# Performance work log

Measured on AMD Instinct MI355X. Metric: run time of the kernel, lower is better.

## Reference

```python
import jax, jax.numpy as jnp
import numpy as np

B, S, D, H = 2, 2048, 1024, 16
Dh = D // H

def setup_inputs() -> dict:
    key = jax.random.key(0)
    ks = jax.random.split(key, 11)
    def lin(k, fan_in):
        bound = 1.0 / np.sqrt(fan_in)
        kw, kb = jax.random.split(k)
        W = jax.random.uniform(kw, (D, D), jnp.float32, -bound, bound)
        b = jax.random.uniform(kb, (D,), jnp.float32, -bound, bound)
        return W, b
    Wq, bq = lin(ks[0], D)
    Wk, bk = lin(ks[1], D)
    Wv, bv = lin(ks[2], D)
    Wo, bo = lin(ks[3], D)
    Q = jax.random.normal(ks[4], (B, S, D), jnp.float32)
    K = jax.random.normal(ks[5], (B, S, D), jnp.float32)
    V = jax.random.normal(ks[6], (B, S, D), jnp.float32)
    return {"Q": Q, "K": K, "V": V, "Wq": Wq, "bq": bq, "Wk": Wk, "bk": bk,
            "Wv": Wv, "bv": bv, "Wo": Wo, "bo": bo}

def _split_heads(x):
    # [B,S,D] -> [B,H,S,Dh]
    b, s, _ = x.shape
    return x.reshape(b, s, H, Dh).transpose(0, 2, 1, 3)

def reference(Q, K, V, Wq, bq, Wk, bk, Wv, bv, Wo, bo):
    q = _split_heads(Q @ Wq.T + bq)
    k = _split_heads(K @ Wk.T + bk)
    v = _split_heads(V @ Wv.T + bv)
    scores = jnp.einsum('bhqd,bhkd->bhqk', q, k) / jnp.sqrt(jnp.float32(Dh))
    attn = jax.nn.softmax(scores, axis=-1)
    out = jnp.einsum('bhqk,bhkd->bhqd', attn, v)  # [B,H,S,Dh]
    out = out.transpose(0, 2, 1, 3).reshape(Q.shape[0], Q.shape[1], D)
    return out @ Wo.T + bo
```

## Files before the change

kernel.cpp:

```cpp
#include <hip/hip_runtime.h>

#define SEQ 2048
#define DMODEL 1024
#define NH 16
#define DH 64

typedef __attribute__((ext_vector_type(8))) short bf16x8;
typedef __attribute__((ext_vector_type(4))) short bf16x4;
typedef __attribute__((ext_vector_type(4))) float floatx4;
typedef __attribute__((ext_vector_type(4))) unsigned short u16x4;
typedef unsigned short u16;
typedef unsigned int u32;

typedef const void __attribute__((address_space(1)))* as1cvp;
typedef void __attribute__((address_space(3)))* as3vp;

__device__ __forceinline__ void glds16(const void* g, void* l) {
    __builtin_amdgcn_global_load_lds((as1cvp)g, (as3vp)l, 16, 0, 0);
}

__device__ __forceinline__ u16 f2bf(float f) {
    union { u32 u; float f; } v; v.f = f;
    return (u16)((v.u + 0x8000u) >> 16);
}

__device__ __forceinline__ u32 pk2(float a, float b) {
    union { u32 u; float f; } x, y; x.f = a; y.f = b;
    u32 xr = x.u + 0x8000u, yr = y.u + 0x8000u;
#if __has_builtin(__builtin_amdgcn_perm)
    return __builtin_amdgcn_perm(yr, xr, 0x07060302u);
#else
    return (xr >> 16) | (yr & 0xffff0000u);
#endif
}

__device__ __forceinline__ float ex2(float x) {
#if __has_builtin(__builtin_amdgcn_exp2f)
    return __builtin_amdgcn_exp2f(x);
#else
    float r; asm("v_exp_f32 %0, %1" : "=v"(r) : "v"(x)); return r;
#endif
}

__device__ __forceinline__ floatx4 mfma16(bf16x4 a, bf16x4 b, floatx4 c) {
#if __has_builtin(__builtin_amdgcn_mfma_f32_16x16x16bf16_1k)
    return __builtin_amdgcn_mfma_f32_16x16x16bf16_1k(a, b, c, 0, 0, 0);
#else
    asm volatile("v_mfma_f32_16x16x16_bf16 %0, %1, %2, %0" : "+v"(c) : "v"(a), "v"(b));
    return c;
#endif
}

__device__ __forceinline__ uint4 cvt8(const float* __restrict__ p) {
    float4 a = *(const float4*)p;
    float4 b = *(const float4*)(p + 4);
    uint4 q;
    q.x = pk2(a.x, a.y); q.y = pk2(a.z, a.w);
    q.z = pk2(b.x, b.y); q.w = pk2(b.z, b.w);
    return q;
}

#define QSCALE 0.18033688011112042f

__global__ __launch_bounds__(256) void cvt_all(
    const float* __restrict__ Q, const float* __restrict__ K, const float* __restrict__ V,
    const float* __restrict__ W0, const float* __restrict__ W1,
    const float* __restrict__ W2, const float* __restrict__ W3,
    u16* __restrict__ Qb, u16* __restrict__ Kb, u16* __restrict__ Vb,
    u16* __restrict__ Wb)
{
    const int y = blockIdx.y;
    const float* src; u16* dst;
    if (y == 0)      { src = Q;  dst = Qb; }
    else if (y == 1) { src = K;  dst = Kb; }
    else if (y == 2) { src = V;  dst = Vb; }
    else {
        if (blockIdx.x >= 512) return;
        src = (y == 3) ? W0 : (y == 4) ? W1 : (y == 5) ? W2 : W3;
        dst = Wb + (size_t)(y - 3) * 1048576;
    }
    size_t i = ((size_t)blockIdx.x * 256 + threadIdx.x) * 8;
    *(uint4*)(dst + i) = cvt8(src + i);
}

__global__ __launch_bounds__(256) void cvt_w(
    const float* __restrict__ W0, const float* __restrict__ W1,
    const float* __restrict__ W2, const float* __restrict__ W3,
    u16* __restrict__ out)
{
    const float* src = (blockIdx.y == 0) ? W0 : (blockIdx.y == 1) ? W1
                     : (blockIdx.y == 2) ? W2 : W3;
    size_t i = ((size_t)blockIdx.x * 256 + threadIdx.x) * 8;
    *(uint4*)(out + (size_t)blockIdx.y * 1048576 + i) = cvt8(src + i);
}

__device__ __forceinline__ void qkv_store(
    int z, u16* __restrict__ outp, int rowg, int col, floatx4 a4, float bv, float sc)
{
    union { u32 w[2]; u16 h[4]; u16x4 v4; } pk;
    pk.w[0] = pk2((a4[0] + bv) * sc, (a4[1] + bv) * sc);
    pk.w[1] = pk2((a4[2] + bv) * sc, (a4[3] + bv) * sc);
    int b = rowg >> 11, s = rowg & 2047, h = col >> 6, d = col & 63;
    if (z < 2) {
#pragma unroll
        for (int r = 0; r < 4; r++)
            outp[((size_t)(b * NH + h) * SEQ + s + r) * DH + d] = pk.h[r];
    } else {
        *(u16x4*)(outp + ((size_t)(b * NH + h) * DH + d) * SEQ + s) = pk.v4;
    }
}

__global__ __launch_bounds__(256) void gemm_qkv_bb(
    const u16* __restrict__ Qb, const u16* __restrict__ Kb, const u16* __restrict__ Vb,
    const u16* __restrict__ Wb,
    const float* __restrict__ b0, const float* __restrict__ b1, const float* __restrict__ b2,
    u16* __restrict__ qo, u16* __restrict__ ko, u16* __restrict__ vto)
{
    __shared__ __align__(16) u16 As[128 * 32];
    __shared__ __align__(16) u16 Bs[128 * 32];
    const int tid = threadIdx.x, l = tid & 63, w = tid >> 6;
    const int lm = l & 15, quad = l >> 4;
    const int wr = (w >> 1) * 64, wc = (w & 1) * 64;
    const int bm = blockIdx.y * 128, bn = blockIdx.x * 128;
    const int z = blockIdx.z;
    const u16* A      = (z == 0) ? Qb : (z == 1) ? Kb : Vb;
    const u16* W      = Wb + (size_t)z * 1048576;
    const float* bias = (z == 0) ? b0 : (z == 1) ? b1 : b2;

    const int srow = tid >> 2, scol = (tid & 3) * 8;

    floatx4 acc[4][4];
#pragma unroll
    for (int i = 0; i < 4; i++)
#pragma unroll
        for (int j = 0; j < 4; j++) acc[i][j] = (floatx4){0.f, 0.f, 0.f, 0.f};

    for (int kt = 0; kt < DMODEL; kt += 32) {
        __syncthreads();
        glds16(A + (size_t)(bm + srow) * DMODEL + kt + scol, As + w * 512);
        glds16(A + (size_t)(bm + 64 + srow) * DMODEL + kt + scol, As + 2048 + w * 512);
        glds16(W + (size_t)(bn + srow) * DMODEL + kt + scol, Bs + w * 512);
        glds16(W + (size_t)(bn + 64 + srow) * DMODEL + kt + scol, Bs + 2048 + w * 512);
        __syncthreads();

        bf16x8 af[4], bfr[4];
#pragma unroll
        for (int mi = 0; mi < 4; mi++)
            af[mi] = *(const bf16x8*)(As + (wr + mi * 16 + lm) * 32 + quad * 8);
#pragma unroll
        for (int ni = 0; ni < 4; ni++)
            bfr[ni] = *(const bf16x8*)(Bs + (wc + ni * 16 + lm) * 32 + quad * 8);
#pragma unroll
        for (int mi = 0; mi < 4; mi++)
#pragma unroll
            for (int ni = 0; ni < 4; ni++)
                acc[mi][ni] = __builtin_amdgcn_mfma_f32_16x16x32_bf16(
                    af[mi], bfr[ni], acc[mi][ni], 0, 0, 0);
    }

    const float sc = (z == 0) ? QSCALE : 1.0f;
    u16* outp = (z == 0) ? qo : (z == 1) ? ko : vto;
#pragma unroll
    for (int ni = 0; ni < 4; ni++) {
        int col = bn + wc + ni * 16 + lm;
        float bv = bias[col];
#pragma unroll
        for (int mi = 0; mi < 4; mi++)
            qkv_store(z, outp, bm + wr + mi * 16 + quad * 4, col, acc[mi][ni], bv, sc);
    }
}

template<bool WBF>
__global__ __launch_bounds__(256) void gemm_qkv(
    const float* __restrict__ Qf, const float* __restrict__ Kf, const float* __restrict__ Vf,
    const void* __restrict__ W0, const void* __restrict__ W1, const void* __restrict__ W2,
    const float* __restrict__ b0, const float* __restrict__ b1, const float* __restrict__ b2,
    u16* __restrict__ qo, u16* __restrict__ ko, u16* __restrict__ vto)
{
    __shared__ __align__(16) u16 As[128 * 32];
    __shared__ __align__(16) u16 Bs[128 * 32];
    const int tid = threadIdx.x, l = tid & 63, w = tid >> 6;
    const int lm = l & 15, quad = l >> 4;
    const int wr = (w >> 1) * 64, wc = (w & 1) * 64;
    const int bm = blockIdx.y * 128, bn = blockIdx.x * 128;
    const int z = blockIdx.z;
    const float* A    = (z == 0) ? Qf : (z == 1) ? Kf : Vf;
    const void* Wp    = (z == 0) ? W0 : (z == 1) ? W1 : W2;
    const float* bias = (z == 0) ? b0 : (z == 1) ? b1 : b2;

    floatx4 acc[4][4];
#pragma unroll
    for (int i = 0; i < 4; i++)
#pragma unroll
        for (int j = 0; j < 4; j++) acc[i][j] = (floatx4){0.f, 0.f, 0.f, 0.f};

    for (int kt = 0; kt < DMODEL; kt += 32) {
        __syncthreads();
#pragma unroll
        for (int j = 0; j < 2; j++) {
            int ch = j * 256 + tid, row = ch >> 2, c = ch & 3;
            *(uint4*)(As + ch * 8) = cvt8(A + (size_t)(bm + row) * DMODEL + kt + c * 8);
        }
        if (WBF) {
            const u16* Wb = (const u16*)Wp;
            glds16(Wb + (size_t)(bn + (tid >> 2)) * DMODEL + kt + (tid & 3) * 8, Bs + w * 512);
            glds16(Wb + (size_t)(bn + 64 + (tid >> 2)) * DMODEL + kt + (tid & 3) * 8, Bs + 2048 + w * 512);
        } else {
            const float* Wf = (const float*)Wp;
#pragma unroll
            for (int j = 0; j < 2; j++) {
                int ch = j * 256 + tid, row = ch >> 2, c = ch & 3;
                *(uint4*)(Bs + ch * 8) = cvt8(Wf + (size_t)(bn + row) * DMODEL + kt + c * 8);
            }
        }
        __syncthreads();

        bf16x8 af[4], bfr[4];
#pragma unroll
        for (int mi = 0; mi < 4; mi++)
            af[mi] = *(const bf16x8*)(As + (wr + mi * 16 + lm) * 32 + quad * 8);
#pragma unroll
        for (int ni = 0; ni < 4; ni++)
            bfr[ni] = *(const bf16x8*)(Bs + (wc + ni * 16 + lm) * 32 + quad * 8);
#pragma unroll
        for (int mi = 0; mi < 4; mi++)
#pragma unroll
            for (int ni = 0; ni < 4; ni++)
                acc[mi][ni] = __builtin_amdgcn_mfma_f32_16x16x32_bf16(
                    af[mi], bfr[ni], acc[mi][ni], 0, 0, 0);
    }

    const float sc = (z == 0) ? QSCALE : 1.0f;
    u16* outp = (z == 0) ? qo : (z == 1) ? ko : vto;
#pragma unroll
    for (int ni = 0; ni < 4; ni++) {
        int col = bn + wc + ni * 16 + lm;
        float bv = bias[col];
#pragma unroll
        for (int mi = 0; mi < 4; mi++)
            qkv_store(z, outp, bm + wr + mi * 16 + quad * 4, col, acc[mi][ni], bv, sc);
    }
}

template<bool WBF>
__global__ __launch_bounds__(256) void gemm_o(
    const u16* __restrict__ A, const void* __restrict__ Wp,
    const float* __restrict__ bias, float* __restrict__ out)
{
    __shared__ __align__(16) u16 As[128 * 32];
    __shared__ __align__(16) u16 Bs[64 * 32];
    const int tid = threadIdx.x, l = tid & 63, w = tid >> 6;
    const int lm = l & 15, quad = l >> 4;
    const int bm = blockIdx.y * 128, bn = blockIdx.x * 64;

    floatx4 acc[2][4];
#pragma unroll
    for (int i = 0; i < 2; i++)
#pragma unroll
        for (int j = 0; j < 4; j++) acc[i][j] = (floatx4){0.f, 0.f, 0.f, 0.f};

    for (int kt = 0; kt < DMODEL; kt += 32) {
        __syncthreads();
        glds16(A + (size_t)(bm + (tid >> 2)) * DMODEL + kt + (tid & 3) * 8, As + w * 512);
        glds16(A + (size_t)(bm + 64 + (tid >> 2)) * DMODEL + kt + (tid & 3) * 8, As + 2048 + w * 512);
        if (WBF) {
            glds16((const u16*)Wp + (size_t)(bn + (tid >> 2)) * DMODEL + kt + (tid & 3) * 8, Bs + w * 512);
        } else {
            *(uint4*)(Bs + tid * 8) =
                cvt8((const float*)Wp + (size_t)(bn + (tid >> 2)) * DMODEL + kt + (tid & 3) * 8);
        }
        __syncthreads();

        bf16x8 af[2], bfr[4];
#pragma unroll
        for (int mi = 0; mi < 2; mi++)
            af[mi] = *(const bf16x8*)(As + (w * 32 + mi * 16 + lm) * 32 + quad * 8);
#pragma unroll
        for (int ni = 0; ni < 4; ni++)
            bfr[ni] = *(const bf16x8*)(Bs + (ni * 16 + lm) * 32 + quad * 8);
#pragma unroll
        for (int mi = 0; mi < 2; mi++)
#pragma unroll
            for (int ni = 0; ni < 4; ni++)
                acc[mi][ni] = __builtin_amdgcn_mfma_f32_16x16x32_bf16(
                    af[mi], bfr[ni], acc[mi][ni], 0, 0, 0);
    }

#pragma unroll
    for (int ni = 0; ni < 4; ni++) {
        int col = bn + ni * 16 + lm;
        float bv = bias[col];
#pragma unroll
        for (int mi = 0; mi < 2; mi++) {
#pragma unroll
            for (int r = 0; r < 4; r++) {
                int rowg = bm + w * 32 + mi * 16 + quad * 4 + r;
                out[(size_t)rowg * DMODEL + col] = acc[mi][ni][r] + bv;
            }
        }
    }
}

#define SP 72
__global__ __launch_bounds__(256, 2) void attn_kernel(
    const u16* __restrict__ q, const u16* __restrict__ k,
    const u16* __restrict__ vt, u16* __restrict__ out)
{
    __shared__ __align__(16) u16 Ks[64 * SP];
    __shared__ __align__(16) u16 Vs[64 * SP];
    const int tid = threadIdx.x, l = tid & 63, w = tid >> 6;
    const int lm = l & 15, quad = l >> 4;
    const int qt = blockIdx.x, bh = blockIdx.y;
    const int b = bh >> 4, h = bh & 15;

    bf16x8 qf[2][2];
#pragma unroll
    for (int nt = 0; nt < 2; nt++) {
        int row = qt * 128 + w * 32 + nt * 16 + lm;
        const u16* qp = q + ((size_t)bh * SEQ + row) * DH;
#pragma unroll
        for (int ks = 0; ks < 2; ks++)
            qf[nt][ks] = *(const bf16x8*)(qp + ks * 32 + quad * 8);
    }

    floatx4 O[4][2];
#pragma unroll
    for (int dt = 0; dt < 4; dt++)
#pragma unroll
        for (int nt = 0; nt < 2; nt++) O[dt][nt] = (floatx4){0.f, 0.f, 0.f, 0.f};
    float mrun[2] = {-1e30f, -1e30f}, lrun[2] = {0.f, 0.f};

    const int srow = tid >> 3, scol = (tid & 7) * 8;
    const int pb0 = ((scol >> 2) & 3) * 16 + (scol >> 4) * 4;
    const u16* kbase = k + (size_t)bh * SEQ * DH;
    const u16* vbase = vt + (size_t)bh * DH * SEQ;
    uint4 kr0, kr1, vr0, vr1;
    kr0 = *(const uint4*)(kbase + (size_t)srow * DH + scol);
    kr1 = *(const uint4*)(kbase + (size_t)(srow + 32) * DH + scol);
    vr0 = *(const uint4*)(vbase + (size_t)srow * SEQ + scol);
    vr1 = *(const uint4*)(vbase + (size_t)(srow + 32) * SEQ + scol);

    for (int t = 0; t < SEQ / 64; t++) {
        __syncthreads();
        *(uint4*)(Ks + srow * SP + scol) = kr0;
        *(uint4*)(Ks + (srow + 32) * SP + scol) = kr1;
        *(uint2*)(Vs + srow * SP + pb0)             = make_uint2(vr0.x, vr0.y);
        *(uint2*)(Vs + srow * SP + pb0 + 16)        = make_uint2(vr0.z, vr0.w);
        *(uint2*)(Vs + (srow + 32) * SP + pb0)      = make_uint2(vr1.x, vr1.y);
        *(uint2*)(Vs + (srow + 32) * SP + pb0 + 16) = make_uint2(vr1.z, vr1.w);
        __syncthreads();
        if (t + 1 < SEQ / 64) {
            const u16* kg = kbase + (size_t)(t + 1) * 64 * DH;
            const u16* vg = vbase + (size_t)(t + 1) * 64;
            kr0 = *(const uint4*)(kg + (size_t)srow * DH + scol);
            kr1 = *(const uint4*)(kg + (size_t)(srow + 32) * DH + scol);
            vr0 = *(const uint4*)(vg + (size_t)srow * SEQ + scol);
            vr1 = *(const uint4*)(vg + (size_t)(srow + 32) * SEQ + scol);
        }

        floatx4 Sc[4][2];
#pragma unroll
        for (int mt = 0; mt < 4; mt++) {
            bf16x8 ka0 = *(const bf16x8*)(Ks + (mt * 16 + lm) * SP + quad * 8);
            bf16x8 ka1 = *(const bf16x8*)(Ks + (mt * 16 + lm) * SP + 32 + quad * 8);
#pragma unroll
            for (int nt = 0; nt < 2; nt++) {
                floatx4 c = (floatx4){0.f, 0.f, 0.f, 0.f};
                c = __builtin_amdgcn_mfma_f32_16x16x32_bf16(ka0, qf[nt][0], c, 0, 0, 0);
                c = __builtin_amdgcn_mfma_f32_16x16x32_bf16(ka1, qf[nt][1], c, 0, 0, 0);
                Sc[mt][nt] = c;
            }
        }

        bf16x4 pb[4][2];
#pragma unroll
        for (int nt = 0; nt < 2; nt++) {
            float m0 = -1e30f;
#pragma unroll
            for (int mt = 0; mt < 4; mt++)
#pragma unroll
                for (int r = 0; r < 4; r++) m0 = fmaxf(m0, Sc[mt][nt][r]);
            m0 = fmaxf(m0, __shfl_xor(m0, 16));
            m0 = fmaxf(m0, __shfl_xor(m0, 32));
            if (!__all(m0 <= mrun[nt] + 8.0f)) {
                float mn = fmaxf(mrun[nt], m0);
                float alpha = ex2(mrun[nt] - mn);
                mrun[nt] = mn;
                lrun[nt] *= alpha;
#pragma unroll
                for (int dt = 0; dt < 4; dt++)
#pragma unroll
                    for (int r = 0; r < 4; r++) O[dt][nt][r] *= alpha;
            }
            const float mn = mrun[nt];
            float s0 = 0.f;
#pragma unroll
            for (int mt = 0; mt < 4; mt++) {
#pragma unroll
                for (int r = 0; r < 4; r++) {
                    float e = ex2(Sc[mt][nt][r] - mn);
                    Sc[mt][nt][r] = e;
                    s0 += e;
                }
                union { u32 w2[2]; bf16x4 v; } pku;
                pku.w2[0] = pk2(Sc[mt][nt][0], Sc[mt][nt][1]);
                pku.w2[1] = pk2(Sc[mt][nt][2], Sc[mt][nt][3]);
                pb[mt][nt] = pku.v;
            }
            s0 += __shfl_xor(s0, 16);
            s0 += __shfl_xor(s0, 32);
            lrun[nt] += s0;
        }

#pragma unroll
        for (int dt = 0; dt < 4; dt++) {
            const u16* vp = Vs + (dt * 16 + lm) * SP + quad * 16;
            bf16x8 v8a = *(const bf16x8*)vp;
            bf16x8 v8b = *(const bf16x8*)(vp + 8);
            bf16x4 va0 = __builtin_shufflevector(v8a, v8a, 0, 1, 2, 3);
            bf16x4 va1 = __builtin_shufflevector(v8a, v8a, 4, 5, 6, 7);
            bf16x4 va2 = __builtin_shufflevector(v8b, v8b, 0, 1, 2, 3);
            bf16x4 va3 = __builtin_shufflevector(v8b, v8b, 4, 5, 6, 7);
            O[dt][0] = mfma16(va0, pb[0][0], O[dt][0]);
            O[dt][1] = mfma16(va0, pb[0][1], O[dt][1]);
            O[dt][0] = mfma16(va1, pb[1][0], O[dt][0]);
            O[dt][1] = mfma16(va1, pb[1][1], O[dt][1]);
            O[dt][0] = mfma16(va2, pb[2][0], O[dt][0]);
            O[dt][1] = mfma16(va2, pb[2][1], O[dt][1]);
            O[dt][0] = mfma16(va3, pb[3][0], O[dt][0]);
            O[dt][1] = mfma16(va3, pb[3][1], O[dt][1]);
        }
    }

#pragma unroll
    for (int nt = 0; nt < 2; nt++) {
        float inv = 1.0f / lrun[nt];
        int s = qt * 128 + w * 32 + nt * 16 + lm;
        u16* op = out + ((size_t)b * SEQ + s) * DMODEL + h * DH;
#pragma unroll
        for (int dt = 0; dt < 4; dt++) {
            union { u32 w2[2]; u16x4 v; } pku;
            pku.w2[0] = pk2(O[dt][nt][0] * inv, O[dt][nt][1] * inv);
            pku.w2[1] = pk2(O[dt][nt][2] * inv, O[dt][nt][3] * inv);
            *(u16x4*)(op + dt * 16 + quad * 4) = pku.v;
        }
    }
}

extern "C" void kernel_launch(void* const* d_in, const int* in_sizes, int n_in,
                              void* d_out, int out_size, void* d_ws, size_t ws_size,
                              hipStream_t stream) {
    (void)in_sizes; (void)n_in; (void)out_size;
    const float* Q  = (const float*)d_in[0];
    const float* K  = (const float*)d_in[1];
    const float* V  = (const float*)d_in[2];
    const float* Wq = (const float*)d_in[3];
    const float* bq = (const float*)d_in[4];
    const float* Wk = (const float*)d_in[5];
    const float* bk = (const float*)d_in[6];
    const float* Wv = (const float*)d_in[7];
    const float* bv = (const float*)d_in[8];
    const float* Wo = (const float*)d_in[9];
    const float* bo = (const float*)d_in[10];

    const size_t NEL = (size_t)2 * NH * SEQ * DH;
    u16* base = (u16*)d_ws;
    dim3 bb(256);

    if (ws_size >= 8 * NEL * 2) {
        u16* Qb   = base;
        u16* Kb   = Qb + NEL;
        u16* Vb   = Kb + NEL;
        u16* Wb   = Vb + NEL;
        u16* qws  = Wb + NEL;
        u16* kws  = qws + NEL;
        u16* vtws = kws + NEL;
        u16* aws  = vtws + NEL;
        cvt_all<<<dim3(2048, 7), bb, 0, stream>>>(Q, K, V, Wq, Wk, Wv, Wo, Qb, Kb, Vb, Wb);
        gemm_qkv_bb<<<dim3(8, 32, 3), bb, 0, stream>>>(
            Qb, Kb, Vb, Wb, bq, bk, bv, qws, kws, vtws);
        attn_kernel<<<dim3(SEQ / 128, 2 * NH), bb, 0, stream>>>(qws, kws, vtws, aws);
        gemm_o<true><<<dim3(16, 32), bb, 0, stream>>>(aws, Wb + 3145728, bo, (float*)d_out);
    } else if (ws_size >= 5 * NEL * 2) {
        u16* Wb = base;
        u16* qws = base + NEL; u16* kws = qws + NEL; u16* vtws = kws + NEL; u16* aws = vtws + NEL;
        cvt_w<<<dim3(512, 4), bb, 0, stream>>>(Wq, Wk, Wv, Wo, Wb);
        gemm_qkv<true><<<dim3(8, 32, 3), bb, 0, stream>>>(
            Q, K, V, Wb, Wb + 1048576, Wb + 2097152, bq, bk, bv, qws, kws, vtws);
        attn_kernel<<<dim3(SEQ / 128, 2 * NH), bb, 0, stream>>>(qws, kws, vtws, aws);
        gemm_o<true><<<dim3(16, 32), bb, 0, stream>>>(aws, Wb + 3145728, bo, (float*)d_out);
    } else {
        u16* qws = base; u16* kws = qws + NEL; u16* vtws = kws + NEL; u16* aws = vtws + NEL;
        gemm_qkv<false><<<dim3(8, 32, 3), bb, 0, stream>>>(
            Q, K, V, Wq, Wk, Wv, bq, bk, bv, qws, kws, vtws);
        attn_kernel<<<dim3(SEQ / 128, 2 * NH), bb, 0, stream>>>(qws, kws, vtws, aws);
        gemm_o<false><<<dim3(16, 32), bb, 0, stream>>>(aws, Wo, bo, (float*)d_out);
    }
}
```

Before: 238.6 us.

## Split attention work across 8 waves per block and compute row sums via MFMA

The attention kernel now launches 512 threads per block, with each wave owning 16 query rows instead of 32. This halves per-thread register state (O, Sc, pb) and raises the occupancy hint to 4 blocks. The softmax row-sum shuffles are replaced by an MFMA against a ones vector that accumulates the denominator in bf16-rounded form, and the max reduction uses three-input max. K/V staging loads per thread halve, but each wave now re-reads the full K/V tiles from LDS for fewer queries, which raises LDS traffic per FLOP.

```diff
diff --git a/kernel.cpp b/kernel.cpp
--- a/kernel.cpp
+++ b/kernel.cpp
@@ -40,6 +40,10 @@
 #else
     float r; asm("v_exp_f32 %0, %1" : "=v"(r) : "v"(x)); return r;
 #endif
+}
+
+__device__ __forceinline__ float max3f(float a, float b, float c) {
+    return fmaxf(fmaxf(a, b), c);
 }
 
 __device__ __forceinline__ floatx4 mfma16(bf16x4 a, bf16x4 b, floatx4 c) {
@@ -302,7 +306,7 @@
 }
 
 #define SP 72
-__global__ __launch_bounds__(256, 2) void attn_kernel(
+__global__ __launch_bounds__(512, 4) void attn_kernel(
     const u16* __restrict__ q, const u16* __restrict__ k,
     const u16* __restrict__ vt, u16* __restrict__ out)
 {
@@ -313,104 +317,88 @@
     const int qt = blockIdx.x, bh = blockIdx.y;
     const int b = bh >> 4, h = bh & 15;
 
-    bf16x8 qf[2][2];
-#pragma unroll
-    for (int nt = 0; nt < 2; nt++) {
-        int row = qt * 128 + w * 32 + nt * 16 + lm;
+    bf16x8 qf[2];
+    {
+        int row = qt * 128 + w * 16 + lm;
         const u16* qp = q + ((size_t)bh * SEQ + row) * DH;
-#pragma unroll
-        for (int ks = 0; ks < 2; ks++)
-            qf[nt][ks] = *(const bf16x8*)(qp + ks * 32 + quad * 8);
-    }
-
-    floatx4 O[4][2];
-#pragma unroll
-    for (int dt = 0; dt < 4; dt++)
-#pragma unroll
-        for (int nt = 0; nt < 2; nt++) O[dt][nt] = (floatx4){0.f, 0.f, 0.f, 0.f};
-    float mrun[2] = {-1e30f, -1e30f}, lrun[2] = {0.f, 0.f};
+        qf[0] = *(const bf16x8*)(qp + quad * 8);
+        qf[1] = *(const bf16x8*)(qp + 32 + quad * 8);
+    }
+
+    floatx4 O[4];
+#pragma unroll
+    for (int dt = 0; dt < 4; dt++) O[dt] = (floatx4){0.f, 0.f, 0.f, 0.f};
+    floatx4 Ol = (floatx4){0.f, 0.f, 0.f, 0.f};
+    float mrun = -1e30f;
+
+    const bf16x4 onesb = {(short)0x3F80, (short)0x3F80, (short)0x3F80, (short)0x3F80};
 
     const int srow = tid >> 3, scol = (tid & 7) * 8;
     const int pb0 = ((scol >> 2) & 3) * 16 + (scol >> 4) * 4;
     const u16* kbase = k + (size_t)bh * SEQ * DH;
     const u16* vbase = vt + (size_t)bh * DH * SEQ;
-    uint4 kr0, kr1, vr0, vr1;
-    kr0 = *(const uint4*)(kbase + (size_t)srow * DH + scol);
-    kr1 = *(const uint4*)(kbase + (size_t)(srow + 32) * DH + scol);
-    vr0 = *(const uint4*)(vbase + (size_t)srow * SEQ + scol);
-    vr1 = *(const uint4*)(vbase + (size_t)(srow + 32) * SEQ + scol);
+    uint4 kr = *(const uint4*)(kbase + (size_t)srow * DH + scol);
+    uint4 vr = *(const uint4*)(vbase + (size_t)srow * SEQ + scol);
 
     for (int t = 0; t < SEQ / 64; t++) {
         __syncthreads();
-        *(uint4*)(Ks + srow * SP + scol) = kr0;
-        *(uint4*)(Ks + (srow + 32) * SP + scol) = kr1;
-        *(uint2*)(Vs + srow * SP + pb0)             = make_uint2(vr0.x, vr0.y);
-        *(uint2*)(Vs + srow * SP + pb0 + 16)        = make_uint2(vr0.z, vr0.w);
-        *(uint2*)(Vs + (srow + 32) * SP + pb0)      = make_uint2(vr1.x, vr1.y);
-        *(uint2*)(Vs + (srow + 32) * SP + pb0 + 16) = make_uint2(vr1.z, vr1.w);
+        *(uint4*)(Ks + srow * SP + scol) = kr;
+        *(uint2*)(Vs + srow * SP + pb0)      = make_uint2(vr.x, vr.y);
+        *(uint2*)(Vs + srow * SP + pb0 + 16) = make_uint2(vr.z, vr.w);
         __syncthreads();
         if (t + 1 < SEQ / 64) {
-            const u16* kg = kbase + (size_t)(t + 1) * 64 * DH;
-            const u16* vg = vbase + (size_t)(t + 1) * 64;
-            kr0 = *(const uint4*)(kg + (size_t)srow * DH + scol);
-            kr1 = *(const uint4*)(kg + (size_t)(srow + 32) * DH + scol);
-            vr0 = *(const uint4*)(vg + (size_t)srow * SEQ + scol);
-            vr1 = *(const uint4*)(vg + (size_t)(srow + 32) * SEQ + scol);
-        }
-
-        floatx4 Sc[4][2];
+            kr = *(const uint4*)(kbase + (size_t)(t + 1) * 64 * DH + (size_t)srow * DH + scol);
+            vr = *(const uint4*)(vbase + (size_t)(t + 1) * 64 + (size_t)srow * SEQ + scol);
+        }
+
+        floatx4 Sc[4];
 #pragma unroll
         for (int mt = 0; mt < 4; mt++) {
             bf16x8 ka0 = *(const bf16x8*)(Ks + (mt * 16 + lm) * SP + quad * 8);
             bf16x8 ka1 = *(const bf16x8*)(Ks + (mt * 16 + lm) * SP + 32 + quad * 8);
-#pragma unroll
-            for (int nt = 0; nt < 2; nt++) {
-                floatx4 c = (floatx4){0.f, 0.f, 0.f, 0.f};
-                c = __builtin_amdgcn_mfma_f32_16x16x32_bf16(ka0, qf[nt][0], c, 0, 0, 0);
-                c = __builtin_amdgcn_mfma_f32_16x16x32_bf16(ka1, qf[nt][1], c, 0, 0, 0);
-                Sc[mt][nt] = c;
-            }
-        }
-
-        bf16x4 pb[4][2];
-#pragma unroll
-        for (int nt = 0; nt < 2; nt++) {
-            float m0 = -1e30f;
-#pragma unroll
-            for (int mt = 0; mt < 4; mt++)
-#pragma unroll
-                for (int r = 0; r < 4; r++) m0 = fmaxf(m0, Sc[mt][nt][r]);
-            m0 = fmaxf(m0, __shfl_xor(m0, 16));
-            m0 = fmaxf(m0, __shfl_xor(m0, 32));
-            if (!__all(m0 <= mrun[nt] + 8.0f)) {
-                float mn = fmaxf(mrun[nt], m0);
-                float alpha = ex2(mrun[nt] - mn);
-                mrun[nt] = mn;
-                lrun[nt] *= alpha;
-#pragma unroll
-                for (int dt = 0; dt < 4; dt++)
-#pragma unroll
-                    for (int r = 0; r < 4; r++) O[dt][nt][r] *= alpha;
-            }
-            const float mn = mrun[nt];
-            float s0 = 0.f;
-#pragma unroll
-            for (int mt = 0; mt < 4; mt++) {
-#pragma unroll
-                for (int r = 0; r < 4; r++) {
-                    float e = ex2(Sc[mt][nt][r] - mn);
-                    Sc[mt][nt][r] = e;
-                    s0 += e;
-                }
-                union { u32 w2[2]; bf16x4 v; } pku;
-                pku.w2[0] = pk2(Sc[mt][nt][0], Sc[mt][nt][1]);
-                pku.w2[1] = pk2(Sc[mt][nt][2], Sc[mt][nt][3]);
-                pb[mt][nt] = pku.v;
-            }
-            s0 += __shfl_xor(s0, 16);
-            s0 += __shfl_xor(s0, 32);
-            lrun[nt] += s0;
-        }
+            floatx4 c = (floatx4){0.f, 0.f, 0.f, 0.f};
+            c = __builtin_amdgcn_mfma_f32_16x16x32_bf16(ka0, qf[0], c, 0, 0, 0);
+            c = __builtin_amdgcn_mfma_f32_16x16x32_bf16(ka1, qf[1], c, 0, 0, 0);
+            Sc[mt] = c;
+        }
+
+        float m0 = max3f(Sc[0][0], Sc[0][1], Sc[0][2]);
+        float m1 = max3f(Sc[0][3], Sc[1][0], Sc[1][1]);
+        float m2 = max3f(Sc[1][2], Sc[1][3], Sc[2][0]);
+        float m3 = max3f(Sc[2][1], Sc[2][2], Sc[2][3]);
+        float m4 = max3f(Sc[3][0], Sc[3][1], Sc[3][2]);
+        m0 = max3f(m0, m1, m2);
+        m0 = max3f(m0, m3, m4);
+        m0 = fmaxf(m0, Sc[3][3]);
+        m0 = fmaxf(m0, __shfl_xor(m0, 16));
+        m0 = fmaxf(m0, __shfl_xor(m0, 32));
+
+        if (!__all(m0 <= mrun + 8.0f)) {
+            float mn = fmaxf(mrun, m0);
+            float alpha = ex2(mrun - mn);
+            mrun = mn;
+#pragma unroll
+            for (int dt = 0; dt < 4; dt++)
+#pragma unroll
+                for (int r = 0; r < 4; r++) O[dt][r] *= alpha;
+            Ol[0] *= alpha;
+        }
+
+        bf16x4 pb[4];
+#pragma unroll
+        for (int mt = 0; mt < 4; mt++) {
+#pragma unroll
+            for (int r = 0; r < 4; r++) Sc[mt][r] = ex2(Sc[mt][r] - mrun);
+            union { u32 w2[2]; bf16x4 v; } pku;
+            pku.w2[0] = pk2(Sc[mt][0], Sc[mt][1]);
+            pku.w2[1] = pk2(Sc[mt][2], Sc[mt][3]);
+            pb[mt] = pku.v;
+        }
+
+        Ol = mfma16(onesb, pb[0], Ol);
+        Ol = mfma16(onesb, pb[1], Ol);
+        Ol = mfma16(onesb, pb[2], Ol);
+        Ol = mfma16(onesb, pb[3], Ol);
 
 #pragma unroll
         for (int dt = 0; dt < 4; dt++) {
@@ -421,29 +409,22 @@
             bf16x4 va1 = __builtin_shufflevector(v8a, v8a, 4, 5, 6, 7);
             bf16x4 va2 = __builtin_shufflevector(v8b, v8b, 0, 1, 2, 3);
             bf16x4 va3 = __builtin_shufflevector(v8b, v8b, 4, 5, 6, 7);
-            O[dt][0] = mfma16(va0, pb[0][0], O[dt][0]);
-            O[dt][1] = mfma16(va0, pb[0][1], O[dt][1]);
-            O[dt][0] = mfma16(va1, pb[1][0], O[dt][0]);
-            O[dt][1] = mfma16(va1, pb[1][1], O[dt][1]);
-            O[dt][0] = mfma16(va2, pb[2][0], O[dt][0]);
-            O[dt][1] = mfma16(va2, pb[2][1], O[dt][1]);
-            O[dt][0] = mfma16(va3, pb[3][0], O[dt][0]);
-            O[dt][1] = mfma16(va3, pb[3][1], O[dt][1]);
-        }
-    }
-
-#pragma unroll
-    for (int nt = 0; nt < 2; nt++) {
-        float inv = 1.0f / lrun[nt];
-        int s = qt * 128 + w * 32 + nt * 16 + lm;
-        u16* op = out + ((size_t)b * SEQ + s) * DMODEL + h * DH;
-#pragma unroll
-        for (int dt = 0; dt < 4; dt++) {
-            union { u32 w2[2]; u16x4 v; } pku;
-            pku.w2[0] = pk2(O[dt][nt][0] * inv, O[dt][nt][1] * inv);
-            pku.w2[1] = pk2(O[dt][nt][2] * inv, O[dt][nt][3] * inv);
-            *(u16x4*)(op + dt * 16 + quad * 4) = pku.v;
-        }
+            O[dt] = mfma16(va0, pb[0], O[dt]);
+            O[dt] = mfma16(va1, pb[1], O[dt]);
+            O[dt] = mfma16(va2, pb[2], O[dt]);
+            O[dt] = mfma16(va3, pb[3], O[dt]);
+        }
+    }
+
+    float inv = 1.0f / Ol[0];
+    int s = qt * 128 + w * 16 + lm;
+    u16* op = out + ((size_t)b * SEQ + s) * DMODEL + h * DH;
+#pragma unroll
+    for (int dt = 0; dt < 4; dt++) {
+        union { u32 w2[2]; u16x4 v; } pku;
+        pku.w2[0] = pk2(O[dt][0] * inv, O[dt][1] * inv);
+        pku.w2[1] = pk2(O[dt][2] * inv, O[dt][3] * inv);
+        *(u16x4*)(op + dt * 16 + quad * 4) = pku.v;
     }
 }
 
@@ -466,6 +447,7 @@
     const size_t NEL = (size_t)2 * NH * SEQ * DH;
     u16* base = (u16*)d_ws;
     dim3 bb(256);
+    dim3 ab(512);
 
     if (ws_size >= 8 * NEL * 2) {
         u16* Qb   = base;
@@ -479,7 +461,7 @@
         cvt_all<<<dim3(2048, 7), bb, 0, stream>>>(Q, K, V, Wq, Wk, Wv, Wo, Qb, Kb, Vb, Wb);
         gemm_qkv_bb<<<dim3(8, 32, 3), bb, 0, stream>>>(
             Qb, Kb, Vb, Wb, bq, bk, bv, qws, kws, vtws);
-        attn_kernel<<<dim3(SEQ / 128, 2 * NH), bb, 0, stream>>>(qws, kws, vtws, aws);
+        attn_kernel<<<dim3(SEQ / 128, 2 * NH), ab, 0, stream>>>(qws, kws, vtws, aws);
         gemm_o<true><<<dim3(16, 32), bb, 0, stream>>>(aws, Wb + 3145728, bo, (float*)d_out);
     } else if (ws_size >= 5 * NEL * 2) {
         u16* Wb = base;
@@ -487,13 +469,13 @@
         cvt_w<<<dim3(512, 4), bb, 0, stream>>>(Wq, Wk, Wv, Wo, Wb);
         gemm_qkv<true><<<dim3(8, 32, 3), bb, 0, stream>>>(
             Q, K, V, Wb, Wb + 1048576, Wb + 2097152, bq, bk, bv, qws, kws, vtws);
-        attn_kernel<<<dim3(SEQ / 128, 2 * NH), bb, 0, stream>>>(qws, kws, vtws, aws);
+        attn_kernel<<<dim3(SEQ / 128, 2 * NH), ab, 0, stream>>>(qws, kws, vtws, aws);
         gemm_o<true><<<dim3(16, 32), bb, 0, stream>>>(aws, Wb + 3145728, bo, (float*)d_out);
     } else {
         u16* qws = base; u16* kws = qws + NEL; u16* vtws = kws + NEL; u16* aws = vtws + NEL;
         gemm_qkv<false><<<dim3(8, 32, 3), bb, 0, stream>>>(
             Q, K, V, Wq, Wk, Wv, bq, bk, bv, qws, kws, vtws);
-        attn_kernel<<<dim3(SEQ / 128, 2 * NH), bb, 0, stream>>>(qws, kws, vtws, aws);
+        attn_kernel<<<dim3(SEQ / 128, 2 * NH), ab, 0, stream>>>(qws, kws, vtws, aws);
         gemm_o<false><<<dim3(16, 32), bb, 0, stream>>>(aws, Wo, bo, (float*)d_out);
     }
 }
```

Result: faster. 231.9 us (-2.8%).

## Split KV sequence across two wave groups in attention with LDS merge

Applied to the files above, without the earlier changes.

The attention block grows to 512 threads. Two groups of four waves each handle half of the key/value sequence for the same 128 query rows, and their partial softmax states are merged through shared memory at the end. The row-sum is now computed with MFMA against a ones vector instead of shuffle reductions. The max reduction uses three-input max, and s_setprio raises priority around the MFMA sections. This aims to raise parallelism and occupancy per query tile, at the cost of an extra LDS combine step, more shared memory and more register pressure under the new launch bounds.

```diff
diff --git a/kernel.cpp b/kernel.cpp
--- a/kernel.cpp
+++ b/kernel.cpp
@@ -40,6 +40,10 @@
 #else
     float r; asm("v_exp_f32 %0, %1" : "=v"(r) : "v"(x)); return r;
 #endif
+}
+
+__device__ __forceinline__ float max3f(float a, float b, float c) {
+    return fmaxf(fmaxf(a, b), c);
 }
 
 __device__ __forceinline__ floatx4 mfma16(bf16x4 a, bf16x4 b, floatx4 c) {
@@ -302,25 +306,27 @@
 }
 
 #define SP 72
-__global__ __launch_bounds__(256, 2) void attn_kernel(
+__global__ __launch_bounds__(512, 4) void attn_kernel(
     const u16* __restrict__ q, const u16* __restrict__ k,
     const u16* __restrict__ vt, u16* __restrict__ out)
 {
-    __shared__ __align__(16) u16 Ks[64 * SP];
-    __shared__ __align__(16) u16 Vs[64 * SP];
+    __shared__ __align__(16) u16 smem[4 * 64 * SP];
     const int tid = threadIdx.x, l = tid & 63, w = tid >> 6;
     const int lm = l & 15, quad = l >> 4;
     const int qt = blockIdx.x, bh = blockIdx.y;
     const int b = bh >> 4, h = bh & 15;
+    const int rg = w & 3, half = w >> 2;
+
+    const u16* Kh = smem + half * (64 * SP);
+    const u16* Vh = smem + (2 + half) * (64 * SP);
 
     bf16x8 qf[2][2];
 #pragma unroll
     for (int nt = 0; nt < 2; nt++) {
-        int row = qt * 128 + w * 32 + nt * 16 + lm;
+        int row = qt * 128 + rg * 32 + nt * 16 + lm;
         const u16* qp = q + ((size_t)bh * SEQ + row) * DH;
-#pragma unroll
-        for (int ks = 0; ks < 2; ks++)
-            qf[nt][ks] = *(const bf16x8*)(qp + ks * 32 + quad * 8);
+        qf[nt][0] = *(const bf16x8*)(qp + quad * 8);
+        qf[nt][1] = *(const bf16x8*)(qp + 32 + quad * 8);
     }
 
     floatx4 O[4][2];
@@ -328,41 +334,49 @@
     for (int dt = 0; dt < 4; dt++)
 #pragma unroll
         for (int nt = 0; nt < 2; nt++) O[dt][nt] = (floatx4){0.f, 0.f, 0.f, 0.f};
-    float mrun[2] = {-1e30f, -1e30f}, lrun[2] = {0.f, 0.f};
+    floatx4 Ol[2] = {(floatx4){0.f,0.f,0.f,0.f}, (floatx4){0.f,0.f,0.f,0.f}};
+    float mrun[2] = {-1e30f, -1e30f};
+
+    const bf16x4 onesb = {(short)0x3F80, (short)0x3F80, (short)0x3F80, (short)0x3F80};
 
     const int srow = tid >> 3, scol = (tid & 7) * 8;
     const int pb0 = ((scol >> 2) & 3) * 16 + (scol >> 4) * 4;
     const u16* kbase = k + (size_t)bh * SEQ * DH;
     const u16* vbase = vt + (size_t)bh * DH * SEQ;
-    uint4 kr0, kr1, vr0, vr1;
-    kr0 = *(const uint4*)(kbase + (size_t)srow * DH + scol);
-    kr1 = *(const uint4*)(kbase + (size_t)(srow + 32) * DH + scol);
-    vr0 = *(const uint4*)(vbase + (size_t)srow * SEQ + scol);
-    vr1 = *(const uint4*)(vbase + (size_t)(srow + 32) * SEQ + scol);
-
-    for (int t = 0; t < SEQ / 64; t++) {
-        __syncthreads();
-        *(uint4*)(Ks + srow * SP + scol) = kr0;
-        *(uint4*)(Ks + (srow + 32) * SP + scol) = kr1;
-        *(uint2*)(Vs + srow * SP + pb0)             = make_uint2(vr0.x, vr0.y);
-        *(uint2*)(Vs + srow * SP + pb0 + 16)        = make_uint2(vr0.z, vr0.w);
-        *(uint2*)(Vs + (srow + 32) * SP + pb0)      = make_uint2(vr1.x, vr1.y);
-        *(uint2*)(Vs + (srow + 32) * SP + pb0 + 16) = make_uint2(vr1.z, vr1.w);
-        __syncthreads();
-        if (t + 1 < SEQ / 64) {
+    uint4 krA = *(const uint4*)(kbase + (size_t)srow * DH + scol);
+    uint4 krB = *(const uint4*)(kbase + (size_t)(1024 + srow) * DH + scol);
+    uint4 vrA = *(const uint4*)(vbase + (size_t)srow * SEQ + scol);
+    uint4 vrB = *(const uint4*)(vbase + (size_t)srow * SEQ + 1024 + scol);
+
+    u16* K0 = smem;
+    u16* K1 = smem + 64 * SP;
+    u16* V0 = smem + 2 * (64 * SP);
+    u16* V1 = smem + 3 * (64 * SP);
+
+    for (int t = 0; t < 16; t++) {
+        __syncthreads();
+        *(uint4*)(K0 + srow * SP + scol) = krA;
+        *(uint4*)(K1 + srow * SP + scol) = krB;
+        *(uint2*)(V0 + srow * SP + pb0)      = make_uint2(vrA.x, vrA.y);
+        *(uint2*)(V0 + srow * SP + pb0 + 16) = make_uint2(vrA.z, vrA.w);
+        *(uint2*)(V1 + srow * SP + pb0)      = make_uint2(vrB.x, vrB.y);
+        *(uint2*)(V1 + srow * SP + pb0 + 16) = make_uint2(vrB.z, vrB.w);
+        __syncthreads();
+        if (t + 1 < 16) {
             const u16* kg = kbase + (size_t)(t + 1) * 64 * DH;
             const u16* vg = vbase + (size_t)(t + 1) * 64;
-            kr0 = *(const uint4*)(kg + (size_t)srow * DH + scol);
-            kr1 = *(const uint4*)(kg + (size_t)(srow + 32) * DH + scol);
-            vr0 = *(const uint4*)(vg + (size_t)srow * SEQ + scol);
-            vr1 = *(const uint4*)(vg + (size_t)(srow + 32) * SEQ + scol);
+            krA = *(const uint4*)(kg + (size_t)srow * DH + scol);
+            krB = *(const uint4*)(kg + (size_t)(1024 + srow) * DH + scol);
+            vrA = *(const uint4*)(vg + (size_t)srow * SEQ + scol);
+            vrB = *(const uint4*)(vg + (size_t)srow * SEQ + 1024 + scol);
         }
 
         floatx4 Sc[4][2];
+        __builtin_amdgcn_s_setprio(1);
 #pragma unroll
         for (int mt = 0; mt < 4; mt++) {
-            bf16x8 ka0 = *(const bf16x8*)(Ks + (mt * 16 + lm) * SP + quad * 8);
-            bf16x8 ka1 = *(const bf16x8*)(Ks + (mt * 16 + lm) * SP + 32 + quad * 8);
+            bf16x8 ka0 = *(const bf16x8*)(Kh + (mt * 16 + lm) * SP + quad * 8);
+            bf16x8 ka1 = *(const bf16x8*)(Kh + (mt * 16 + lm) * SP + 32 + quad * 8);
 #pragma unroll
             for (int nt = 0; nt < 2; nt++) {
                 floatx4 c = (floatx4){0.f, 0.f, 0.f, 0.f};
@@ -371,50 +385,56 @@
                 Sc[mt][nt] = c;
             }
         }
+        __builtin_amdgcn_s_setprio(0);
 
         bf16x4 pb[4][2];
 #pragma unroll
         for (int nt = 0; nt < 2; nt++) {
-            float m0 = -1e30f;
-#pragma unroll
-            for (int mt = 0; mt < 4; mt++)
-#pragma unroll
-                for (int r = 0; r < 4; r++) m0 = fmaxf(m0, Sc[mt][nt][r]);
+            float m0 = max3f(Sc[0][nt][0], Sc[0][nt][1], Sc[0][nt][2]);
+            float m1 = max3f(Sc[0][nt][3], Sc[1][nt][0], Sc[1][nt][1]);
+            float m2 = max3f(Sc[1][nt][2], Sc[1][nt][3], Sc[2][nt][0]);
+            float m3 = max3f(Sc[2][nt][1], Sc[2][nt][2], Sc[2][nt][3]);
+            float m4 = max3f(Sc[3][nt][0], Sc[3][nt][1], Sc[3][nt][2]);
+            m0 = max3f(m0, m1, m2);
+            m0 = max3f(m0, m3, m4);
+            m0 = fmaxf(m0, Sc[3][nt][3]);
             m0 = fmaxf(m0, __shfl_xor(m0, 16));
             m0 = fmaxf(m0, __shfl_xor(m0, 32));
+
             if (!__all(m0 <= mrun[nt] + 8.0f)) {
                 float mn = fmaxf(mrun[nt], m0);
                 float alpha = ex2(mrun[nt] - mn);
                 mrun[nt] = mn;
-                lrun[nt] *= alpha;
 #pragma unroll
                 for (int dt = 0; dt < 4; dt++)
 #pragma unroll
                     for (int r = 0; r < 4; r++) O[dt][nt][r] *= alpha;
+                Ol[nt][0] *= alpha;
             }
             const float mn = mrun[nt];
-            float s0 = 0.f;
 #pragma unroll
             for (int mt = 0; mt < 4; mt++) {
 #pragma unroll
-                for (int r = 0; r < 4; r++) {
-                    float e = ex2(Sc[mt][nt][r] - mn);
-                    Sc[mt][nt][r] = e;
-                    s0 += e;
-                }
+                for (int r = 0; r < 4; r++) Sc[mt][nt][r] = ex2(Sc[mt][nt][r] - mn);
                 union { u32 w2[2]; bf16x4 v; } pku;
                 pku.w2[0] = pk2(Sc[mt][nt][0], Sc[mt][nt][1]);
                 pku.w2[1] = pk2(Sc[mt][nt][2], Sc[mt][nt][3]);
                 pb[mt][nt] = pku.v;
             }
-            s0 += __shfl_xor(s0, 16);
-            s0 += __shfl_xor(s0, 32);
-            lrun[nt] += s0;
+        }
+
+        __builtin_amdgcn_s_setprio(1);
+#pragma unroll
+        for (int nt = 0; nt < 2; nt++) {
+            Ol[nt] = mfma16(onesb, pb[0][nt], Ol[nt]);
+            Ol[nt] = mfma16(onesb, pb[1][nt], Ol[nt]);
+            Ol[nt] = mfma16(onesb, pb[2][nt], Ol[nt]);
+            Ol[nt] = mfma16(onesb, pb[3][nt], Ol[nt]);
         }
 
 #pragma unroll
         for (int dt = 0; dt < 4; dt++) {
-            const u16* vp = Vs + (dt * 16 + lm) * SP + quad * 16;
+            const u16* vp = Vh + (dt * 16 + lm) * SP + quad * 16;
             bf16x8 v8a = *(const bf16x8*)vp;
             bf16x8 v8b = *(const bf16x8*)(vp + 8);
             bf16x4 va0 = __builtin_shufflevector(v8a, v8a, 0, 1, 2, 3);
@@ -430,19 +450,47 @@
             O[dt][0] = mfma16(va3, pb[3][0], O[dt][0]);
             O[dt][1] = mfma16(va3, pb[3][1], O[dt][1]);
         }
-    }
-
-#pragma unroll
-    for (int nt = 0; nt < 2; nt++) {
-        float inv = 1.0f / lrun[nt];
-        int s = qt * 128 + w * 32 + nt * 16 + lm;
-        u16* op = out + ((size_t)b * SEQ + s) * DMODEL + h * DH;
-#pragma unroll
-        for (int dt = 0; dt < 4; dt++) {
-            union { u32 w2[2]; u16x4 v; } pku;
-            pku.w2[0] = pk2(O[dt][nt][0] * inv, O[dt][nt][1] * inv);
-            pku.w2[1] = pk2(O[dt][nt][2] * inv, O[dt][nt][3] * inv);
-            *(u16x4*)(op + dt * 16 + quad * 4) = pku.v;
+        __builtin_amdgcn_s_setprio(0);
+    }
+
+    __syncthreads();
+    float* obuf  = (float*)smem;
+    float* mlbuf = (float*)smem + 8192;
+    if (w >= 4) {
+#pragma unroll
+        for (int nt = 0; nt < 2; nt++) {
+            float* ob = obuf + (((rg * 64 + l) * 2 + nt) << 4);
+#pragma unroll
+            for (int dt = 0; dt < 4; dt++)
+                *(floatx4*)(ob + dt * 4) = O[dt][nt];
+            *(float2*)(mlbuf + ((rg * 64 + l) * 2 + nt) * 2) =
+                make_float2(mrun[nt], Ol[nt][0]);
+        }
+    }
+    __syncthreads();
+    if (w < 4) {
+#pragma unroll
+        for (int nt = 0; nt < 2; nt++) {
+            float* ob = obuf + (((rg * 64 + l) * 2 + nt) << 4);
+            float2 ml = *(float2*)(mlbuf + ((rg * 64 + l) * 2 + nt) * 2);
+            float mA = mrun[nt], lA = Ol[nt][0];
+            float mB = ml.x, lB = ml.y;
+            float mm = fmaxf(mA, mB);
+            float eA = ex2(mA - mm), eB = ex2(mB - mm);
+            float inv = 1.0f / (lA * eA + lB * eB);
+            float wA = eA * inv, wB = eB * inv;
+            int s = qt * 128 + rg * 32 + nt * 16 + lm;
+            u16* op = out + ((size_t)b * SEQ + s) * DMODEL + h * DH;
+#pragma unroll
+            for (int dt = 0; dt < 4; dt++) {
+                floatx4 Ob = *(const floatx4*)(ob + dt * 4);
+                union { u32 w2[2]; u16x4 v; } pku;
+                pku.w2[0] = pk2(O[dt][nt][0] * wA + Ob[0] * wB,
+                                O[dt][nt][1] * wA + Ob[1] * wB);
+                pku.w2[1] = pk2(O[dt][nt][2] * wA + Ob[2] * wB,
+                                O[dt][nt][3] * wA + Ob[3] * wB);
+                *(u16x4*)(op + dt * 16 + quad * 4) = pku.v;
+            }
         }
     }
 }
@@ -466,6 +514,7 @@
     const size_t NEL = (size_t)2 * NH * SEQ * DH;
     u16* base = (u16*)d_ws;
     dim3 bb(256);
+    dim3 ab(512);
 
     if (ws_size >= 8 * NEL * 2) {
         u16* Qb   = base;
@@ -479,7 +528,7 @@
         cvt_all<<<dim3(2048, 7), bb, 0, stream>>>(Q, K, V, Wq, Wk, Wv, Wo, Qb, Kb, Vb, Wb);
         gemm_qkv_bb<<<dim3(8, 32, 3), bb, 0, stream>>>(
             Qb, Kb, Vb, Wb, bq, bk, bv, qws, kws, vtws);
-        attn_kernel<<<dim3(SEQ / 128, 2 * NH), bb, 0, stream>>>(qws, kws, vtws, aws);
+        attn_kernel<<<dim3(SEQ / 128, 2 * NH), ab, 0, stream>>>(qws, kws, vtws, aws);
         gemm_o<true><<<dim3(16, 32), bb, 0, stream>>>(aws, Wb + 3145728, bo, (float*)d_out);
     } else if (ws_size >= 5 * NEL * 2) {
         u16* Wb = base;
@@ -487,13 +536,13 @@
         cvt_w<<<dim3(512, 4), bb, 0, stream>>>(Wq, Wk, Wv, Wo, Wb);
         gemm_qkv<true><<<dim3(8, 32, 3), bb, 0, stream>>>(
             Q, K, V, Wb, Wb + 1048576, Wb + 2097152, bq, bk, bv, qws, kws, vtws);
-        attn_kernel<<<dim3(SEQ / 128, 2 * NH), bb, 0, stream>>>(qws, kws, vtws, aws);
+        attn_kernel<<<dim3(SEQ / 128, 2 * NH), ab, 0, stream>>>(qws, kws, vtws, aws);
         gemm_o<true><<<dim3(16, 32), bb, 0, stream>>>(aws, Wb + 3145728, bo, (float*)d_out);
     } else {
         u16* qws = base; u16* kws = qws + NEL; u16* vtws = kws + NEL; u16* aws = vtws + NEL;
         gemm_qkv<false><<<dim3(8, 32, 3), bb, 0, stream>>>(
             Q, K, V, Wq, Wk, Wv, bq, bk, bv, qws, kws, vtws);
-        attn_kernel<<<dim3(SEQ / 128, 2 * NH), bb, 0, stream>>>(qws, kws, vtws, aws);
+        attn_kernel<<<dim3(SEQ / 128, 2 * NH), ab, 0, stream>>>(qws, kws, vtws, aws);
         gemm_o<false><<<dim3(16, 32), bb, 0, stream>>>(aws, Wo, bo, (float*)d_out);
     }
 }
```

New measurement: 231.6 us. -2.9%, faster.
